# Performance work log

Measured on AMD Instinct MI355X. Metric: run time of the kernel, lower is better.

The kernel has to match this reference:

```python
import jax, jax.numpy as jnp
import numpy as np

N_NODES = 50000
N_EDGES = 640000
H_DIM = 128


def setup_inputs() -> dict:
    key = jax.random.key(0)
    k1, k2, k3, k4 = jax.random.split(key, 4)
    node_feat = jax.random.normal(k1, (N_NODES, H_DIM), dtype=jnp.float32)
    src = jax.random.randint(k2, (N_EDGES,), 0, N_NODES, dtype=jnp.int64)
    dst = jax.random.randint(k3, (N_EDGES,), 0, N_NODES, dtype=jnp.int64)
    # glorot-uniform kernel, zero bias (as in the original initializers)
    limit = np.sqrt(6.0 / (2 * H_DIM + H_DIM)).astype(np.float32)
    W = jax.random.uniform(k4, (2 * H_DIM, H_DIM), minval=-limit, maxval=limit, dtype=jnp.float32)
    b = jnp.zeros((H_DIM,), dtype=jnp.float32)
    return {"node_feat": node_feat, "src": src, "dst": dst, "W": W, "b": b}


def reference(node_feat, src, dst, W, b):
    # per-edge message: concat(h[src], h[dst]) -> linear  : [E, 2d] @ [2d, d]
    msg = jnp.concatenate([node_feat[src], node_feat[dst]], axis=-1)
    edge_feat = msg @ W + b  # [E, d]
    # scatter-sum over destination nodes (zero for in-degree-0 nodes, as DGL update_all)
    agg = jax.ops.segment_sum(edge_feat, dst, num_segments=node_feat.shape[0])  # [N, d]
    # node apply: sigmoid(aggregated msg) + softplus(old h)
    return jax.nn.sigmoid(agg) + jax.nn.softplus(node_feat)
```

## Files before the change

kernel.cpp:

```cpp
#include <hip/hip_runtime.h>
#include <math.h>

#define HD 128
#define CAP 32
#define OVCAP 8192
#define NPB 16
#define RPT 8

typedef __attribute__((ext_vector_type(8))) short bf16x8;
typedef __attribute__((ext_vector_type(4))) float f32x4;

__device__ inline short f2bf(float x) {
    union { float f; unsigned u; } v; v.f = x;
    unsigned r = v.u + 0x7fff + ((v.u >> 16) & 1);
    return (short)(r >> 16);
}
__device__ inline float bf2f(short x) {
    union { unsigned u; float f; } v;
    v.u = ((unsigned)(unsigned short)x) << 16;
    return v.f;
}

#define LOG2E 1.4426950408889634f
#define LN2   0.6931471805599453f

__device__ inline float fast_sigmoid(float x) {
    return __builtin_amdgcn_rcpf(1.0f + __builtin_amdgcn_exp2f(-LOG2E * x));
}
__device__ inline float fast_softplus(float x) {
    float t = __builtin_amdgcn_exp2f(-LOG2E * fabsf(x));
    return fmaxf(x, 0.0f) + LN2 * __builtin_amdgcn_logf(1.0f + t);
}

__device__ inline void accum8(float* a, const uint4 u) {
    a[0] += __uint_as_float(u.x << 16);
    a[1] += __uint_as_float(u.x & 0xffff0000u);
    a[2] += __uint_as_float(u.y << 16);
    a[3] += __uint_as_float(u.y & 0xffff0000u);
    a[4] += __uint_as_float(u.z << 16);
    a[5] += __uint_as_float(u.z & 0xffff0000u);
    a[6] += __uint_as_float(u.w << 16);
    a[7] += __uint_as_float(u.w & 0xffff0000u);
}


__global__ __launch_bounds__(256) void prep0(
    const float* __restrict__ W, short* __restrict__ WtG,
    int* __restrict__ cnt, int* __restrict__ ov_cnt, int n_nodes)
{
    const int tid = blockIdx.x * 256 + threadIdx.x;
    const int total = gridDim.x * 256;
    for (int i = tid; i < n_nodes; i += total) cnt[i] = 0;
    if (tid == 0) *ov_cnt = 0;
    for (int i = tid; i < 256 * 128; i += total) {
        int j = i >> 7, k = i & 127;
        float w = (j < HD) ? W[k * HD + j] : W[(HD + k) * HD + (j - HD)];
        WtG[i] = f2bf(w);
    }
}

__global__ __launch_bounds__(256) void fill_buckets(
    const int* __restrict__ src, const int* __restrict__ dst,
    int* __restrict__ cnt, unsigned short* __restrict__ bkt,
    unsigned* __restrict__ ov, int* __restrict__ ov_cnt, int n_edges)
{
    int e = blockIdx.x * 256 + threadIdx.x;
    if (e < n_edges) {
        int d = dst[e], s = src[e];
        int pos = atomicAdd(&cnt[d], 1);
        if (pos < CAP) bkt[(size_t)d * CAP + pos] = (unsigned short)s;
        else {
            int op = atomicAdd(ov_cnt, 1);
            if (op < OVCAP) ov[op] = ((unsigned)d << 16) | (unsigned)s;
        }
    }
}


__global__ __launch_bounds__(256) void prep_gemm(
    const float* __restrict__ h,
    const short* __restrict__ WtG,
    const float* __restrict__ bias,
    short* __restrict__ m1b,
    short* __restrict__ m2b,
    int n_nodes)
{
    __shared__ short sb[2][2][16][72];

    const int lane = threadIdx.x & 63;
    const int wv = threadIdx.x >> 6;
    const int half = wv & 1;
    const int ch = wv >> 1;
    const int c0 = ch * 64;
    const int row = lane & 15;
    const int g = lane >> 4;
    const int mBlk = blockIdx.x * 64;

    bf16x8 B[4][4];
    #pragma unroll
    for (int jt = 0; jt < 4; ++jt) {
        const short* wj = WtG + (size_t)(half * HD + c0 + jt * 16 + row) * HD + g * 8;
        #pragma unroll
        for (int kf = 0; kf < 4; ++kf)
            B[jt][kf] = *(const bf16x8*)(wj + kf * 32);
    }
    float bc[4];
    #pragma unroll
    for (int jt = 0; jt < 4; ++jt) bc[jt] = half ? bias[c0 + jt * 16 + row] : 0.f;

    short* const dstp = half ? m2b : m1b;

    float4 af[8];
    {
        int mA = mBlk + row; if (mA > n_nodes - 1) mA = n_nodes - 1;
        #pragma unroll
        for (int kf = 0; kf < 4; ++kf) {
            af[2 * kf]     = *(const float4*)(h + (size_t)mA * HD + kf * 32 + g * 8);
            af[2 * kf + 1] = *(const float4*)(h + (size_t)mA * HD + kf * 32 + g * 8 + 4);
        }
    }

    #pragma unroll
    for (int tt = 0; tt < 4; ++tt) {
        const int m0 = mBlk + tt * 16;

        bf16x8 a[4];
        #pragma unroll
        for (int kf = 0; kf < 4; ++kf) {
            float4 x = af[2 * kf], y = af[2 * kf + 1];
            bf16x8 t = { f2bf(x.x), f2bf(x.y), f2bf(x.z), f2bf(x.w),
                         f2bf(y.x), f2bf(y.y), f2bf(y.z), f2bf(y.w) };
            a[kf] = t;
        }
        if (tt < 3) {
            int mN = m0 + 16 + row; if (mN > n_nodes - 1) mN = n_nodes - 1;
            #pragma unroll
            for (int kf = 0; kf < 4; ++kf) {
                af[2 * kf]     = *(const float4*)(h + (size_t)mN * HD + kf * 32 + g * 8);
                af[2 * kf + 1] = *(const float4*)(h + (size_t)mN * HD + kf * 32 + g * 8 + 4);
            }
        }

        f32x4 acc[4];
        #pragma unroll
        for (int jt = 0; jt < 4; ++jt) acc[jt] = (f32x4){0.f, 0.f, 0.f, 0.f};
        #pragma unroll
        for (int jt = 0; jt < 4; ++jt)
            #pragma unroll
            for (int kf = 0; kf < 4; ++kf)
                acc[jt] = __builtin_amdgcn_mfma_f32_16x16x32_bf16(a[kf], B[jt][kf], acc[jt], 0, 0, 0);

        #pragma unroll
        for (int jt = 0; jt < 4; ++jt)
            #pragma unroll
            for (int r = 0; r < 4; ++r)
                sb[half][ch][g * 4 + r][jt * 16 + row] = f2bf(acc[jt][r] + bc[jt]);
        asm volatile("s_waitcnt lgkmcnt(0)" ::: "memory");
        #pragma unroll
        for (int ps = 0; ps < 2; ++ps) {
            int rr = ps * 8 + (lane >> 3);
            int c8 = lane & 7;
            int n = m0 + rr;
            bf16x8 v = *(const bf16x8*)&sb[half][ch][rr][c8 * 8];
            if (n < n_nodes)
                *(bf16x8*)(dstp + (size_t)n * HD + c0 + c8 * 8) = v;
        }
    }
}


__global__ __launch_bounds__(256) void gather_ep(
    const short* __restrict__ m1b, const int* __restrict__ cnt,
    const unsigned short* __restrict__ bkt,
    const unsigned* __restrict__ ov, const int* __restrict__ ov_cnt,
    const short* __restrict__ m2b,
    const float* __restrict__ h, float* __restrict__ out, int n_nodes)
{
    int g = (blockIdx.x * 256 + threadIdx.x) >> 4;
    int lane = threadIdx.x & 15;
    if (g >= n_nodes) return;
    const int degree = cnt[g];
    const int end = (degree < CAP) ? degree : CAP;
    const unsigned short* bl = bkt + (size_t)g * CAP;
    const size_t lo = (size_t)(lane * 8);

    float a0[8], a1[8];
    #pragma unroll
    for (int q = 0; q < 8; ++q) { a0[q] = 0.f; a1[q] = 0.f; }

    if (end > 0) {
        const int lastv = bl[end - 1];
        const uint4* bl4 = (const uint4*)bl;
        for (int base = 0; base < end; base += 8) {
            uint4 iv = bl4[base >> 3];
            int id8[8];
            id8[0] = iv.x & 0xffff; id8[1] = iv.x >> 16;
            id8[2] = iv.y & 0xffff; id8[3] = iv.y >> 16;
            id8[4] = iv.z & 0xffff; id8[5] = iv.z >> 16;
            id8[6] = iv.w & 0xffff; id8[7] = iv.w >> 16;
            #pragma unroll
            for (int j = 0; j < 8; ++j)
                if (base + j >= end) id8[j] = lastv;
            uint4 v[8];
            #pragma unroll
            for (int j = 0; j < 8; ++j)
                v[j] = *(const uint4*)(m1b + (size_t)id8[j] * HD + lo);
            #pragma unroll
            for (int j = 0; j < 8; ++j) {
                if (base + j < end) accum8((j & 1) ? a1 : a0, v[j]);
            }
        }
    }

    if (degree > CAP) {
        int oc = *ov_cnt; if (oc > OVCAP) oc = OVCAP;
        for (int i = 0; i < oc; ++i) {
            unsigned v = ov[i];
            if ((int)(v >> 16) == g) {
                uint4 vv = *(const uint4*)(m1b + (size_t)(v & 0xffffu) * HD + lo);
                accum8(a0, vv);
            }
        }
    }

    const float dg = (float)degree;
    uint4 mv = *(const uint4*)(m2b + (size_t)g * HD + lo);
    float mr[8];
    mr[0] = __uint_as_float(mv.x << 16); mr[1] = __uint_as_float(mv.x & 0xffff0000u);
    mr[2] = __uint_as_float(mv.y << 16); mr[3] = __uint_as_float(mv.y & 0xffff0000u);
    mr[4] = __uint_as_float(mv.z << 16); mr[5] = __uint_as_float(mv.z & 0xffff0000u);
    mr[6] = __uint_as_float(mv.w << 16); mr[7] = __uint_as_float(mv.w & 0xffff0000u);

    const float4* ph = (const float4*)(h + (size_t)g * HD + lo);
    float4 ha = ph[0], hb4 = ph[1];
    float hr[8] = { ha.x, ha.y, ha.z, ha.w, hb4.x, hb4.y, hb4.z, hb4.w };

    float o[8];
    #pragma unroll
    for (int q = 0; q < 8; ++q) {
        float agg = (a0[q] + a1[q]) + dg * mr[q];
        o[q] = fast_sigmoid(agg) + fast_softplus(hr[q]);
    }
    float4* po = (float4*)(out + (size_t)g * HD + lo);
    po[0] = (float4){o[0], o[1], o[2], o[3]};
    po[1] = (float4){o[4], o[5], o[6], o[7]};
}


__global__ __launch_bounds__(256) void zero_i32(int* __restrict__ p, int n)
{
    int i = blockIdx.x * 256 + threadIdx.x;
    if (i < n) p[i] = 0;
}

__global__ __launch_bounds__(256) void wt_convert(
    const float* __restrict__ W, short* __restrict__ Wt)
{
    int idx = blockIdx.x * 256 + threadIdx.x;
    int j = idx >> 8;
    int k = idx & 255;
    Wt[idx] = f2bf(W[k * HD + j]);
}

__global__ __launch_bounds__(256) void mpnn_scatter(
    const float* __restrict__ h, const int* __restrict__ src,
    const int* __restrict__ dst, float* __restrict__ S,
    int* __restrict__ deg, int n_edges)
{
    int gid = blockIdx.x * 256 + threadIdx.x;
    int e = gid >> 5;
    if (e >= n_edges) return;
    int lane = gid & 31;
    int s = src[e], d = dst[e];
    float4 v = *(const float4*)(h + (size_t)s * HD + lane * 4);
    float* srow = S + (size_t)d * HD + lane * 4;
    atomicAdd(srow + 0, v.x);
    atomicAdd(srow + 1, v.y);
    atomicAdd(srow + 2, v.z);
    atomicAdd(srow + 3, v.w);
    if (lane == 0) atomicAdd(deg + d, 1);
}

__global__ __launch_bounds__(256) void mpnn_node_mfma(
    const float* __restrict__ h,
    const short* __restrict__ Wt,
    const float* __restrict__ bias,
    const int* __restrict__ deg,
    float* __restrict__ S,
    int n_nodes)
{
    const int lane = threadIdx.x & 63;
    const int wv = threadIdx.x >> 6;
    const int m0 = blockIdx.x * 32 + (wv >> 1) * 16;
    const int c0 = (wv & 1) * 64;
    if (m0 >= n_nodes) return;
    const int row = lane & 15;
    const int g = lane >> 4;

    const int nBase = m0 + g * 4;
    float dgO[4], hv[4][4], bc[4];
    #pragma unroll
    for (int r = 0; r < 4; ++r) {
        int n = nBase + r;
        int nc = (n < n_nodes) ? n : (n_nodes - 1);
        dgO[r] = (float)deg[nc];
        #pragma unroll
        for (int jt = 0; jt < 4; ++jt)
            hv[jt][r] = h[(size_t)nc * HD + c0 + jt * 16 + row];
    }
    #pragma unroll
    for (int jt = 0; jt < 4; ++jt) bc[jt] = bias[c0 + jt * 16 + row];

    int mA = m0 + row;
    if (mA > n_nodes - 1) mA = n_nodes - 1;
    const float dgA = (float)deg[mA];

    bf16x8 a[8];
    #pragma unroll
    for (int kf = 0; kf < 4; ++kf) {
        const float4* p = (const float4*)(S + (size_t)mA * HD + kf * 32 + g * 8);
        float4 x = p[0], y = p[1];
        bf16x8 t = { f2bf(x.x), f2bf(x.y), f2bf(x.z), f2bf(x.w),
                     f2bf(y.x), f2bf(y.y), f2bf(y.z), f2bf(y.w) };
        a[kf] = t;
    }
    #pragma unroll
    for (int kf = 0; kf < 4; ++kf) {
        const float4* p = (const float4*)(h + (size_t)mA * HD + kf * 32 + g * 8);
        float4 x = p[0], y = p[1];
        bf16x8 t = { f2bf(dgA * x.x), f2bf(dgA * x.y), f2bf(dgA * x.z), f2bf(dgA * x.w),
                     f2bf(dgA * y.x), f2bf(dgA * y.y), f2bf(dgA * y.z), f2bf(dgA * y.w) };
        a[4 + kf] = t;
    }

    f32x4 acc[4];
    #pragma unroll
    for (int jt = 0; jt < 4; ++jt) acc[jt] = (f32x4){0.f, 0.f, 0.f, 0.f};

    #pragma unroll
    for (int jt = 0; jt < 4; ++jt) {
        const short* wj = Wt + (size_t)(c0 + jt * 16 + row) * 256 + g * 8;
        #pragma unroll
        for (int kf = 0; kf < 8; ++kf) {
            bf16x8 bf = *(const bf16x8*)(wj + kf * 32);
            acc[jt] = __builtin_amdgcn_mfma_f32_16x16x32_bf16(a[kf], bf, acc[jt], 0, 0, 0);
        }
    }

    #pragma unroll
    for (int jt = 0; jt < 4; ++jt) {
        const int col = c0 + jt * 16 + row;
        #pragma unroll
        for (int r = 0; r < 4; ++r) {
            int n = nBase + r;
            if (n < n_nodes) {
                float agg = acc[jt][r] + dgO[r] * bc[jt];
                S[(size_t)n * HD + col] = fast_sigmoid(agg) + fast_softplus(hv[jt][r]);
            }
        }
    }
}

__global__ __launch_bounds__(256) void mpnn_node_f32(
    const float* __restrict__ h, const float* __restrict__ W,
    const float* __restrict__ b, const int* __restrict__ deg,
    float* __restrict__ S, int n_nodes)
{
    const int j = threadIdx.x & (HD - 1);
    const int g = threadIdx.x >> 7;
    const int n0 = blockIdx.x * NPB + g * RPT;

    float accS[RPT], accH[RPT];
    #pragma unroll
    for (int r = 0; r < RPT; ++r) { accS[r] = 0.f; accH[r] = 0.f; }

    int rmax = n_nodes - n0;
    if (rmax > RPT) rmax = RPT;
    if (rmax < 0) rmax = 0;

    for (int k = 0; k < HD; k += 4) {
        float w0 = W[(k + 0) * HD + j], w1 = W[(k + 1) * HD + j];
        float w2 = W[(k + 2) * HD + j], w3 = W[(k + 3) * HD + j];
        #pragma unroll
        for (int r = 0; r < RPT; ++r) if (r < rmax) {
            float4 a = *(const float4*)(S + (size_t)(n0 + r) * HD + k);
            accS[r] = fmaf(a.x, w0, fmaf(a.y, w1, fmaf(a.z, w2, fmaf(a.w, w3, accS[r]))));
        }
    }
    for (int k = 0; k < HD; k += 4) {
        float w0 = W[(HD + k + 0) * HD + j], w1 = W[(HD + k + 1) * HD + j];
        float w2 = W[(HD + k + 2) * HD + j], w3 = W[(HD + k + 3) * HD + j];
        #pragma unroll
        for (int r = 0; r < RPT; ++r) if (r < rmax) {
            float4 a = *(const float4*)(h + (size_t)(n0 + r) * HD + k);
            accH[r] = fmaf(a.x, w0, fmaf(a.y, w1, fmaf(a.z, w2, fmaf(a.w, w3, accH[r]))));
        }
    }
    __syncthreads();
    #pragma unroll
    for (int r = 0; r < RPT; ++r) if (r < rmax) {
        int n = n0 + r;
        float dg = (float)deg[n];
        float agg = accS[r] + dg * (accH[r] + b[j]);
        float hvv = h[(size_t)n * HD + j];
        S[(size_t)n * HD + j] = fast_sigmoid(agg) + fast_softplus(hvv);
    }
}

extern "C" void kernel_launch(void* const* d_in, const int* in_sizes, int n_in,
                              void* d_out, int out_size, void* d_ws, size_t ws_size,
                              hipStream_t stream)
{
    const float* h   = (const float*)d_in[0];
    const int*   src = (const int*)d_in[1];
    const int*   dst = (const int*)d_in[2];
    const float* W   = (const float*)d_in[3];
    const float* b   = (const float*)d_in[4];
    float* S = (float*)d_out;

    const int n_nodes = in_sizes[0] / HD;
    const int n_edges = in_sizes[1];
    const int WT_INTS = 2 * HD * HD / 2;

    char* p = (char*)d_ws;
    auto align16 = [](char* q) { return (char*)(((uintptr_t)q + 15) & ~(uintptr_t)15); };
    p = align16(p); int* cnt = (int*)p;               p += (size_t)n_nodes * 4;
    p = align16(p); unsigned short* bkt = (unsigned short*)p; p += (size_t)n_nodes * CAP * 2;
    p = align16(p); short* WtG = (short*)p;           p += (size_t)256 * HD * 2;
    p = align16(p); unsigned* ov = (unsigned*)p;      p += (size_t)OVCAP * 4;
    p = align16(p); int* ov_cnt = (int*)p;            p += 16;
    p = align16(p); short* m1b = (short*)p;           p += (size_t)n_nodes * HD * 2;
    p = align16(p); short* m2b = (short*)p;           p += (size_t)n_nodes * HD * 2;
    const size_t need_top = (size_t)(p - (char*)d_ws);

    const size_t need_mid = ((size_t)n_nodes + WT_INTS + 8) * sizeof(int);

    if (n_nodes <= 65535 && ws_size >= need_top) {
        prep0<<<256, 256, 0, stream>>>(W, WtG, cnt, ov_cnt, n_nodes);

        fill_buckets<<<(n_edges + 255) / 256, 256, 0, stream>>>(
            src, dst, cnt, bkt, ov, ov_cnt, n_edges);

        const int pblocks = (n_nodes + 63) / 64;
        prep_gemm<<<pblocks, 256, 0, stream>>>(h, WtG, b, m1b, m2b, n_nodes);

        const int gblocks = (int)(((long long)n_nodes * 16 + 255) / 256);
        gather_ep<<<gblocks, 256, 0, stream>>>(m1b, cnt, bkt, ov, ov_cnt,
                                               m2b, h, S, n_nodes);
    } else if (ws_size >= need_mid) {
        int* deg2  = (int*)d_ws;
        short* Wt2 = (short*)(deg2 + n_nodes);
        hipMemsetAsync(d_out, 0, (size_t)n_nodes * HD * sizeof(float), stream);
        zero_i32<<<(n_nodes + 255) / 256, 256, 0, stream>>>(deg2, n_nodes);
        wt_convert<<<(2 * HD * HD) / 256, 256, 0, stream>>>(W, Wt2);
        const int sblocks = (int)(((long long)n_edges * 32 + 255) / 256);
        mpnn_scatter<<<sblocks, 256, 0, stream>>>(h, src, dst, S, deg2, n_edges);
        const int mblocks = (n_nodes + 31) / 32;
        mpnn_node_mfma<<<mblocks, 256, 0, stream>>>(h, Wt2, b, deg2, S, n_nodes);
    } else {
        int* deg2 = (int*)d_ws;
        hipMemsetAsync(d_out, 0, (size_t)n_nodes * HD * sizeof(float), stream);
        zero_i32<<<(n_nodes + 255) / 256, 256, 0, stream>>>(deg2, n_nodes);
        const int sblocks = (int)(((long long)n_edges * 32 + 255) / 256);
        mpnn_scatter<<<sblocks, 256, 0, stream>>>(h, src, dst, S, deg2, n_edges);
        const int nblocks = (n_nodes + NPB - 1) / NPB;
        mpnn_node_f32<<<nblocks, 256, 0, stream>>>(h, W, b, deg2, S, n_nodes);
    }
}
```

Baseline: 110.8 us.

## Replace global-atomic bucket fill with two-pass LDS-binned partition

Edge bucketing by destination now runs as two passes instead of one global atomic per edge. The first pass has 256 producer blocks that bin their edge chunk into 512-node bins in shared memory. The second pass has one block per bin that builds the per-node CAP buckets in LDS and writes them out with vector stores. This drops the per-node count zeroing and the scattered global atomics. In exchange it adds a kernel launch, an intermediate buffer round-trip, a serial per-thread loop in partB, and a limit on the number of bins.

```diff
diff --git a/kernel.cpp b/kernel.cpp
--- a/kernel.cpp
+++ b/kernel.cpp
@@ -4,6 +4,10 @@
 #define HD 128
 #define CAP 32
 #define OVCAP 8192
+#define NPROD 256
+#define PBCAP 64
+#define BINSZ 512
+#define MAXBINS 112
 #define NPB 16
 #define RPT 8
 
@@ -14,11 +18,6 @@
     union { float f; unsigned u; } v; v.f = x;
     unsigned r = v.u + 0x7fff + ((v.u >> 16) & 1);
     return (short)(r >> 16);
-}
-__device__ inline float bf2f(short x) {
-    union { unsigned u; float f; } v;
-    v.u = ((unsigned)(unsigned short)x) << 16;
-    return v.f;
 }
 
 #define LOG2E 1.4426950408889634f
@@ -46,12 +45,11 @@
 
 __global__ __launch_bounds__(256) void prep0(
     const float* __restrict__ W, short* __restrict__ WtG,
-    int* __restrict__ cnt, int* __restrict__ ov_cnt, int n_nodes)
+    int* __restrict__ ovA_cnt, int* __restrict__ ovB_cnt)
 {
     const int tid = blockIdx.x * 256 + threadIdx.x;
     const int total = gridDim.x * 256;
-    for (int i = tid; i < n_nodes; i += total) cnt[i] = 0;
-    if (tid == 0) *ov_cnt = 0;
+    if (tid == 0) { *ovA_cnt = 0; *ovB_cnt = 0; }
     for (int i = tid; i < 256 * 128; i += total) {
         int j = i >> 7, k = i & 127;
         float w = (j < HD) ? W[k * HD + j] : W[(HD + k) * HD + (j - HD)];
@@ -59,19 +57,105 @@
     }
 }
 
-__global__ __launch_bounds__(256) void fill_buckets(
+__global__ __launch_bounds__(256) void partA(
     const int* __restrict__ src, const int* __restrict__ dst,
+    unsigned* __restrict__ pb_buf,
+    int* __restrict__ pb_cnt,
+    unsigned* __restrict__ ovA, int* __restrict__ ovA_cnt,
+    int n_edges, int nbins)
+{
+    __shared__ unsigned buf[MAXBINS][PBCAP];
+    __shared__ int bcnt[MAXBINS];
+
+    const int t = threadIdx.x;
+    for (int i = t; i < nbins; i += 256) bcnt[i] = 0;
+    __syncthreads();
+
+    const int chunk = (n_edges + NPROD - 1) / NPROD;
+    int e0 = blockIdx.x * chunk;
+    int e1 = e0 + chunk; if (e1 > n_edges) e1 = n_edges;
+
+    for (int e = e0 + t; e < e1; e += 256) {
+        int d = dst[e], s = src[e];
+        int bin = d >> 9;
+        unsigned pk = ((unsigned)d << 16) | (unsigned)s;
+        int pos = atomicAdd(&bcnt[bin], 1);
+        if (pos < PBCAP) buf[bin][pos] = pk;
+        else {
+            int op = atomicAdd(ovA_cnt, 1);
+            if (op < OVCAP) ovA[op] = pk;
+        }
+    }
+    __syncthreads();
+
+    unsigned* myb = pb_buf + (size_t)blockIdx.x * nbins * PBCAP;
+    int* myc = pb_cnt + (size_t)blockIdx.x * nbins;
+    for (int b = 0; b < nbins; ++b) {
+        int c = bcnt[b]; if (c > PBCAP) c = PBCAP;
+        if (t < c) myb[(size_t)b * PBCAP + t] = buf[b][t];
+        if (t == 0) myc[b] = c;
+    }
+}
+
+__global__ __launch_bounds__(256) void partB(
+    const unsigned* __restrict__ pb_buf, const int* __restrict__ pb_cnt,
+    const unsigned* __restrict__ ovA, const int* __restrict__ ovA_cnt,
+    unsigned* __restrict__ ovB, int* __restrict__ ovB_cnt,
     int* __restrict__ cnt, unsigned short* __restrict__ bkt,
-    unsigned* __restrict__ ov, int* __restrict__ ov_cnt, int n_edges)
-{
-    int e = blockIdx.x * 256 + threadIdx.x;
-    if (e < n_edges) {
-        int d = dst[e], s = src[e];
-        int pos = atomicAdd(&cnt[d], 1);
-        if (pos < CAP) bkt[(size_t)d * CAP + pos] = (unsigned short)s;
-        else {
-            int op = atomicAdd(ov_cnt, 1);
-            if (op < OVCAP) ov[op] = ((unsigned)d << 16) | (unsigned)s;
+    int n_nodes, int nbins)
+{
+    __shared__ unsigned short lbkt[BINSZ][CAP];
+    __shared__ int lcnt[BINSZ];
+
+    const int t = threadIdx.x;
+    const int bin = blockIdx.x;
+    const int base = bin * BINSZ;
+
+    for (int i = t; i < BINSZ; i += 256) lcnt[i] = 0;
+    __syncthreads();
+
+    {
+        int c = pb_cnt[(size_t)t * nbins + bin];
+        const unsigned* seg = pb_buf + ((size_t)t * nbins + bin) * PBCAP;
+        for (int i = 0; i < c; ++i) {
+            unsigned e = seg[i];
+            int dl = (int)(e >> 16) - base;
+            int pos = atomicAdd(&lcnt[dl], 1);
+            if (pos < CAP) lbkt[dl][pos] = (unsigned short)(e & 0xffffu);
+            else {
+                int op = atomicAdd(ovB_cnt, 1);
+                if (op < OVCAP) ovB[op] = e;
+            }
+        }
+    }
+    {
+        int oc = *ovA_cnt; if (oc > OVCAP) oc = OVCAP;
+        for (int i = t; i < oc; i += 256) {
+            unsigned e = ovA[i];
+            int d = (int)(e >> 16);
+            if ((d >> 9) == bin) {
+                int dl = d - base;
+                int pos = atomicAdd(&lcnt[dl], 1);
+                if (pos < CAP) lbkt[dl][pos] = (unsigned short)(e & 0xffffu);
+                else {
+                    int op = atomicAdd(ovB_cnt, 1);
+                    if (op < OVCAP) ovB[op] = e;
+                }
+            }
+        }
+    }
+    __syncthreads();
+
+    for (int g0 = t; g0 < BINSZ; g0 += 256) {
+        int g = base + g0;
+        if (g < n_nodes) {
+            cnt[g] = lcnt[g0];
+            uint4* dstp = (uint4*)(bkt + (size_t)g * CAP);
+            const uint4* srcp = (const uint4*)&lbkt[g0][0];
+            dstp[0] = srcp[0];
+            dstp[1] = srcp[1];
+            dstp[2] = srcp[2];
+            dstp[3] = srcp[3];
         }
     }
 }
@@ -421,31 +505,38 @@
     const int n_nodes = in_sizes[0] / HD;
     const int n_edges = in_sizes[1];
     const int WT_INTS = 2 * HD * HD / 2;
+    const int nbins = (n_nodes + BINSZ - 1) / BINSZ;
 
     char* p = (char*)d_ws;
     auto align16 = [](char* q) { return (char*)(((uintptr_t)q + 15) & ~(uintptr_t)15); };
-    p = align16(p); int* cnt = (int*)p;               p += (size_t)n_nodes * 4;
+    p = align16(p); int* cnt = (int*)p;                p += (size_t)n_nodes * 4;
     p = align16(p); unsigned short* bkt = (unsigned short*)p; p += (size_t)n_nodes * CAP * 2;
-    p = align16(p); short* WtG = (short*)p;           p += (size_t)256 * HD * 2;
-    p = align16(p); unsigned* ov = (unsigned*)p;      p += (size_t)OVCAP * 4;
-    p = align16(p); int* ov_cnt = (int*)p;            p += 16;
-    p = align16(p); short* m1b = (short*)p;           p += (size_t)n_nodes * HD * 2;
-    p = align16(p); short* m2b = (short*)p;           p += (size_t)n_nodes * HD * 2;
+    p = align16(p); short* WtG = (short*)p;            p += (size_t)256 * HD * 2;
+    p = align16(p); unsigned* pb_buf = (unsigned*)p;   p += (size_t)NPROD * nbins * PBCAP * 4;
+    p = align16(p); int* pb_cnt = (int*)p;             p += (size_t)NPROD * nbins * 4;
+    p = align16(p); unsigned* ovA = (unsigned*)p;      p += (size_t)OVCAP * 4;
+    p = align16(p); unsigned* ovB = (unsigned*)p;      p += (size_t)OVCAP * 4;
+    p = align16(p); int* ovA_cnt = (int*)p;            p += 16;
+    p = align16(p); int* ovB_cnt = (int*)p;            p += 16;
+    p = align16(p); short* m1b = (short*)p;            p += (size_t)n_nodes * HD * 2;
+    p = align16(p); short* m2b = (short*)p;            p += (size_t)n_nodes * HD * 2;
     const size_t need_top = (size_t)(p - (char*)d_ws);
 
     const size_t need_mid = ((size_t)n_nodes + WT_INTS + 8) * sizeof(int);
 
-    if (n_nodes <= 65535 && ws_size >= need_top) {
-        prep0<<<256, 256, 0, stream>>>(W, WtG, cnt, ov_cnt, n_nodes);
-
-        fill_buckets<<<(n_edges + 255) / 256, 256, 0, stream>>>(
-            src, dst, cnt, bkt, ov, ov_cnt, n_edges);
+    if (n_nodes <= BINSZ * MAXBINS && n_nodes <= 65535 && ws_size >= need_top) {
+        prep0<<<128, 256, 0, stream>>>(W, WtG, ovA_cnt, ovB_cnt);
+
+        partA<<<NPROD, 256, 0, stream>>>(src, dst, pb_buf, pb_cnt,
+                                         ovA, ovA_cnt, n_edges, nbins);
+        partB<<<nbins, 256, 0, stream>>>(pb_buf, pb_cnt, ovA, ovA_cnt,
+                                         ovB, ovB_cnt, cnt, bkt, n_nodes, nbins);
 
         const int pblocks = (n_nodes + 63) / 64;
         prep_gemm<<<pblocks, 256, 0, stream>>>(h, WtG, b, m1b, m2b, n_nodes);
 
         const int gblocks = (int)(((long long)n_nodes * 16 + 255) / 256);
-        gather_ep<<<gblocks, 256, 0, stream>>>(m1b, cnt, bkt, ov, ov_cnt,
+        gather_ep<<<gblocks, 256, 0, stream>>>(m1b, cnt, bkt, ovB, ovB_cnt,
                                                m2b, h, S, n_nodes);
     } else if (ws_size >= need_mid) {
         int* deg2  = (int*)d_ws;
```

Result: faster. 99.48 us (-10.2%).
